# Kernel tuning notes

Hardware: AMD Instinct MI355X
Metric: run time of the kernel (lower is better)

The kernel has to match this reference:

```python
import jax, jax.numpy as jnp
import numpy as np

C_CURV = 1.0      # manifold curvature c (= k in the torch code)
EPS = 1e-15
PROJ_EPS = 1e-5   # standard Poincare ball boundary eps for manifold.proj


def _clamp_abs(x, eps=EPS):
    return jnp.maximum(jnp.abs(x), eps) * jnp.sign(x)


def setup_inputs() -> dict:
    key = jax.random.key(0)
    k1, k2, k3 = jax.random.split(key, 3)
    B, D, C = 4096, 1024, 4096
    c = C_CURV
    x = jax.random.normal(k1, (B, D), dtype=jnp.float32)
    # reset_parameters(): a ~ N(0, D^-0.5 / sqrt(c)); p ~ N(0, 0.1) clipped to norm 0.9/sqrt(c)
    a = jax.random.normal(k2, (C, D), dtype=jnp.float32) * (D ** -0.5 / c ** 0.5)
    p = jax.random.normal(k3, (C, D), dtype=jnp.float32) * 0.1
    p_norm = jnp.linalg.norm(p, axis=1, keepdims=True)
    max_norm = 0.9 / jnp.sqrt(jnp.float32(c))
    p = p * jnp.minimum(max_norm / p_norm, 1.0)
    return {"x": x, "a": a, "p": p}


def _forward(x, a, p):
    k = jnp.float32(C_CURV)
    sqrt_k = jnp.sqrt(k)

    # manifold.proj: clip x to the open ball of radius (1 - eps)/sqrt(c)
    xn = jnp.maximum(jnp.linalg.norm(x, axis=-1, keepdims=True), EPS)
    maxn = (1.0 - PROJ_EPS) / sqrt_k
    x = jnp.where(xn > maxn, x * (maxn / xn), x)

    # Rank-structured Mobius addition: diff = mobius_add(-p, x) factors as
    #   diff[b,c,:] = (A[b,c] * (-p[c]) + Bc[c] * x[b]) / den[b,c]
    x2 = jnp.sum(x * x, axis=-1)          # [B]
    p2 = jnp.sum(p * p, axis=-1)          # [C]
    px = jnp.einsum('bd,cd->bc', x, p)    # [B,C]  <p_c, x_b>
    xa = jnp.einsum('bd,cd->bc', x, a)    # [B,C]  <a_c, x_b>
    pa = jnp.sum(p * a, axis=-1)          # [C]    <p_c, a_c>
    a_norm = jnp.sqrt(jnp.sum(a * a, axis=-1))  # [C]

    A = 1.0 - 2.0 * k * px + k * x2[:, None]                       # [B,C]
    Bc = 1.0 - k * p2                                              # [C]
    den = jnp.maximum(1.0 - 2.0 * k * px + (k * k) * x2[:, None] * p2[None, :], EPS)

    diff_norm2 = jnp.maximum(
        (A * A * p2[None, :] + (Bc * Bc)[None, :] * x2[:, None] - 2.0 * A * Bc[None, :] * px)
        / (den * den), EPS)                                        # [B,C]
    sc_diff_a = (-A * pa[None, :] + Bc[None, :] * xa) / den        # [B,C], signed

    num = 2.0 * sc_diff_a
    denom = _clamp_abs((1.0 + k * diff_norm2) * a_norm[None, :])
    distance = jnp.arcsinh(sqrt_k * num / denom) / sqrt_k
    return -distance  # logits [B,C]


def reference(x, a, p):
    return _forward(x, a, p)
```

## Files before the change

kernel.cpp:

```cpp
#include <hip/hip_runtime.h>
#include <hip/hip_bf16.h>
#include <math.h>


#define EPSF 1e-15f
#define MAXN 0.99999f

constexpr int Bdim = 4096;
constexpr int Ddim = 1024;
constexpr int Cdim = 4096;

typedef __bf16 bf16x8 __attribute__((ext_vector_type(8)));
typedef float  f32x4  __attribute__((ext_vector_type(4)));
typedef unsigned short u16;

__device__ __forceinline__ u16 f2bf(float f) {
  __hip_bfloat16 h = __float2bfloat16(f);
  return *reinterpret_cast<const u16*>(&h);
}

__device__ __forceinline__ void gl_lds16(const u16* g, u16* l) {
  __builtin_amdgcn_global_load_lds(
      (const __attribute__((address_space(1))) void*)g,
      (__attribute__((address_space(3))) void*)l, 16, 0, 0);
}


__global__ __launch_bounds__(256) void prep_x(const float* __restrict__ x,
                                              u16* __restrict__ xb,
                                              float* __restrict__ x2o) {
  const int b = blockIdx.x, t = threadIdx.x;
  float4 v = ((const float4*)(x + (size_t)b * Ddim))[t];
  float s = v.x * v.x + v.y * v.y + v.z * v.z + v.w * v.w;
  __shared__ float red[4];
#pragma unroll
  for (int o = 32; o > 0; o >>= 1) s += __shfl_down(s, o);
  if ((t & 63) == 0) red[t >> 6] = s;
  __syncthreads();
  s = red[0] + red[1] + red[2] + red[3];
  float norm  = sqrtf(s);
  float xn    = fmaxf(norm, EPSF);
  float scale = (xn > MAXN) ? (MAXN / xn) : 1.0f;
  if (t == 0) x2o[b] = s * scale * scale;
  ushort4 o4;
  o4.x = f2bf(v.x * scale); o4.y = f2bf(v.y * scale);
  o4.z = f2bf(v.z * scale); o4.w = f2bf(v.w * scale);
  ((ushort4*)(xb + (size_t)b * Ddim))[t] = o4;
}

__global__ __launch_bounds__(256) void prep_pa(const float* __restrict__ a,
                                               const float* __restrict__ p,
                                               u16* __restrict__ pab,
                                               float* __restrict__ p2o,
                                               float* __restrict__ pao,
                                               float* __restrict__ ano) {
  const int c = blockIdx.x, t = threadIdx.x;
  float4 av = ((const float4*)(a + (size_t)c * Ddim))[t];
  float4 pv = ((const float4*)(p + (size_t)c * Ddim))[t];
  float sp2 = pv.x * pv.x + pv.y * pv.y + pv.z * pv.z + pv.w * pv.w;
  float spa = pv.x * av.x + pv.y * av.y + pv.z * av.z + pv.w * av.w;
  float sa2 = av.x * av.x + av.y * av.y + av.z * av.z + av.w * av.w;
  __shared__ float red[12];
#pragma unroll
  for (int o = 32; o > 0; o >>= 1) {
    sp2 += __shfl_down(sp2, o);
    spa += __shfl_down(spa, o);
    sa2 += __shfl_down(sa2, o);
  }
  if ((t & 63) == 0) { int w = t >> 6; red[w] = sp2; red[4 + w] = spa; red[8 + w] = sa2; }
  __syncthreads();
  if (t == 0) {
    p2o[c] = red[0] + red[1] + red[2] + red[3];
    pao[c] = red[4] + red[5] + red[6] + red[7];
    ano[c] = sqrtf(red[8] + red[9] + red[10] + red[11]);
  }
  const int prP = ((c >> 4) << 5) + (c & 15);
  ushort4 oa, op;
  oa.x = f2bf(av.x); oa.y = f2bf(av.y); oa.z = f2bf(av.z); oa.w = f2bf(av.w);
  op.x = f2bf(pv.x); op.y = f2bf(pv.y); op.z = f2bf(pv.z); op.w = f2bf(pv.w);
  ((ushort4*)(pab + (size_t)prP * Ddim))[t]        = op;
  ((ushort4*)(pab + (size_t)(prP + 16) * Ddim))[t] = oa;
}


#define SBAR0() __builtin_amdgcn_sched_barrier(0)
#define GATE8() asm volatile("s_waitcnt vmcnt(8)" ::: "memory")
#define GATE4() asm volatile("s_waitcnt vmcnt(4)" ::: "memory")
#define GATE0() asm volatile("s_waitcnt vmcnt(0)" ::: "memory")

__global__ __launch_bounds__(512, 2) void gemm_ep(
    const u16* __restrict__ xb, const u16* __restrict__ pab,
    const float* __restrict__ x2g, const float* __restrict__ p2g,
    const float* __restrict__ pag, const float* __restrict__ ang,
    float* __restrict__ out) {
  __shared__ u16 Xs[4][8192];
  __shared__ u16 PAs[4][8192];

  const int t = threadIdx.x;

  const int flat  = blockIdx.y * 32 + blockIdx.x;
  const int swz   = (flat & 7) * 64 + (flat >> 3);
  const int chunk = swz >> 6;
  const int local = swz & 63;
  const int bx = chunk * 4 + (local & 3);
  const int by = local >> 2;

  const int lane = t & 63;
  const int wid  = t >> 6;
  const int wr   = wid >> 2;
  const int wc   = wid & 3;

  const int r0  = t >> 2;
  const int sw8 = ((t & 3) ^ ((r0 >> 1) & 3)) * 8;
  const u16* xsrc  = xb  + (size_t)(by * 256 + r0) * Ddim + sw8;
  const u16* pasrc = pab + (size_t)(bx * 256 + r0) * Ddim + sw8;
  const int t8 = t * 8;
  const size_t half = (size_t)128 * Ddim;

  const int arow = wr * 128 + (lane & 15);
  const int brow = wc * 64  + (lane & 15);
  const int aoff = arow * 32 + (((lane >> 4) ^ ((arow >> 1) & 3)) * 8);
  const int boff = brow * 32 + (((lane >> 4) ^ ((brow >> 1) & 3)) * 8);

  f32x4 acc[8][4];
  const f32x4 zero = {0.f, 0.f, 0.f, 0.f};
#pragma unroll
  for (int m = 0; m < 8; ++m)
#pragma unroll
    for (int n = 0; n < 4; ++n) acc[m][n] = zero;

#define MROW(M, AV) do {                                                     \
    acc[M][0] = __builtin_amdgcn_mfma_f32_16x16x32_bf16(AV, bv0, acc[M][0], 0, 0, 0); \
    acc[M][1] = __builtin_amdgcn_mfma_f32_16x16x32_bf16(AV, bv1, acc[M][1], 0, 0, 0); \
    acc[M][2] = __builtin_amdgcn_mfma_f32_16x16x32_bf16(AV, bv2, acc[M][2], 0, 0, 0); \
    acc[M][3] = __builtin_amdgcn_mfma_f32_16x16x32_bf16(AV, bv3, acc[M][3], 0, 0, 0); \
  } while (0)

#define TILE(BI, DOSTAGE, GATE) do {                                  \
    GATE;                                                             \
    __builtin_amdgcn_s_barrier();                                     \
    SBAR0();                                                          \
    if (DOSTAGE) {                                                    \
      u16* Xw  = (u16*)&Xs[((BI)+3)&3][0];                            \
      u16* PAw = (u16*)&PAs[((BI)+3)&3][0];                           \
      gl_lds16(xgp,        Xw + t8);                                  \
      gl_lds16(xgp + half, Xw + 4096 + t8);                           \
      gl_lds16(pgp,        PAw + t8);                                 \
      gl_lds16(pgp + half, PAw + 4096 + t8);                          \
      xgp += 32; pgp += 32;                                           \
    }                                                                 \
    const u16* Xr  = &Xs[(BI)][0];                                    \
    const u16* PAr = &PAs[(BI)][0];                                   \
    bf16x8 bv0 = *(const bf16x8*)&PAr[boff];                          \
    bf16x8 bv1 = *(const bf16x8*)&PAr[boff + 512];                    \
    bf16x8 bv2 = *(const bf16x8*)&PAr[boff + 1024];                   \
    bf16x8 bv3 = *(const bf16x8*)&PAr[boff + 1536];                   \
    bf16x8 a0 = *(const bf16x8*)&Xr[aoff];                            \
    bf16x8 a1 = *(const bf16x8*)&Xr[aoff + 512];                      \
    bf16x8 a2 = *(const bf16x8*)&Xr[aoff + 1024];                     \
    bf16x8 a3 = *(const bf16x8*)&Xr[aoff + 1536];                     \
    asm volatile("s_waitcnt lgkmcnt(0)" ::: "memory");                \
    SBAR0();                                                          \
    __builtin_amdgcn_s_setprio(1);                                    \
    MROW(0, a0); MROW(1, a1);                                         \
    SBAR0();                                                          \
    a0 = *(const bf16x8*)&Xr[aoff + 2048];                            \
    a1 = *(const bf16x8*)&Xr[aoff + 2560];                            \
    SBAR0();                                                          \
    MROW(2, a2); MROW(3, a3);                                         \
    SBAR0();                                                          \
    a2 = *(const bf16x8*)&Xr[aoff + 3072];                            \
    a3 = *(const bf16x8*)&Xr[aoff + 3584];                            \
    SBAR0();                                                          \
    asm volatile("s_waitcnt lgkmcnt(2)" ::: "memory");                \
    SBAR0();                                                          \
    MROW(4, a0); MROW(5, a1);                                         \
    asm volatile("s_waitcnt lgkmcnt(0)" ::: "memory");                \
    SBAR0();                                                          \
    MROW(6, a2); MROW(7, a3);                                         \
    __builtin_amdgcn_s_setprio(0);                                    \
  } while (0)

#pragma unroll
  for (int T = 0; T < 3; ++T) {
    u16* Xw  = (u16*)&Xs[T][0];
    u16* PAw = (u16*)&PAs[T][0];
    gl_lds16(xsrc  + T * 32,        Xw + t8);
    gl_lds16(xsrc  + T * 32 + half, Xw + 4096 + t8);
    gl_lds16(pasrc + T * 32,        PAw + t8);
    gl_lds16(pasrc + T * 32 + half, PAw + 4096 + t8);
  }
  const u16* xgp = xsrc  + 96;
  const u16* pgp = pasrc + 96;

  for (int g = 0; g < 7; ++g) {
    TILE(0, 1, GATE8());
    TILE(1, 1, GATE8());
    TILE(2, 1, GATE8());
    TILE(3, 1, GATE8());
  }
  TILE(0, 1, GATE8());
  TILE(1, 0, GATE8());
  TILE(2, 0, GATE4());
  TILE(3, 0, GATE0());

#undef TILE
#undef MROW

#pragma unroll
  for (int m = 0; m < 8; ++m) {
    const int rl0 = by * 256 + wr * 128 + m * 16 + (lane >> 4) * 4;
    float x2r[4];
#pragma unroll
    for (int j = 0; j < 4; ++j) x2r[j] = x2g[rl0 + j];
#pragma unroll
    for (int g = 0; g < 2; ++g) {
      const int cl = (bx * 8 + wc * 2 + g) * 16 + (lane & 15);
      const float p2c = p2g[cl];
      const float pac = pag[cl];
      const float anc = ang[cl];
      const float Bcc = 1.0f - p2c;
      f32x4 px4 = acc[m][2 * g];
      f32x4 xa4 = acc[m][2 * g + 1];
#pragma unroll
      for (int j = 0; j < 4; ++j) {
        const float px = px4[j];
        const float xa = xa4[j];
        const float Av  = 1.0f - 2.0f * px + x2r[j];
        const float den = fmaxf(1.0f - 2.0f * px + x2r[j] * p2c, EPSF);
        const float dn2 = fmaxf((Av * Av * p2c + Bcc * Bcc * x2r[j] - 2.0f * Av * Bcc * px) / (den * den), EPSF);
        const float sc  = (Bcc * xa - Av * pac) / den;
        const float dv  = fmaxf((1.0f + dn2) * anc, EPSF);
        const float z   = (2.0f * sc) / dv;
        const float z2 = z * z;
        float r;
        if (z2 > 0.04f) r = asinhf(z);
        else            r = z * (1.0f - z2 * (1.0f / 6.0f) + z2 * z2 * 0.075f);
        out[(size_t)rl0 * Cdim + j * Cdim + cl] = -r;
      }
    }
  }
}

extern "C" void kernel_launch(void* const* d_in, const int* in_sizes, int n_in,
                              void* d_out, int out_size, void* d_ws, size_t ws_size,
                              hipStream_t stream) {
  const float* x = (const float*)d_in[0];
  const float* a = (const float*)d_in[1];
  const float* p = (const float*)d_in[2];
  float* out = (float*)d_out;

  char* ws = (char*)d_ws;
  u16* xb  = (u16*)(ws);
  u16* pab = (u16*)(ws + (size_t)8 * 1024 * 1024);
  float* x2 = (float*)(ws + (size_t)24 * 1024 * 1024);
  float* p2 = x2 + Bdim;
  float* pa = p2 + Cdim;
  float* an = pa + Cdim;

  prep_x <<<Bdim, 256, 0, stream>>>(x, xb, x2);
  prep_pa<<<Cdim, 256, 0, stream>>>(a, p, pab, p2, pa, an);
  gemm_ep<<<dim3(32, 16), 512, 0, stream>>>(xb, pab, x2, p2, pa, an, out);
}
```

Before: 124.6 us.

## Double-buffer LDS fragments in registers and prefetch next tile mid-compute

The GEMM main loop now keeps two register fragment sets. Halfway through each tile's MFMA sequence it loads the next tile's B fragments and first four A fragments from LDS, so LDS read latency overlaps matrix math instead of stalling at the start of each tile. The global-load gate is relaxed from vmcnt(8) to vmcnt(4), with a one-time prologue wait before the loop. Most explicit sched_barrier and lgkmcnt waits are removed, which leaves wait placement to the compiler. The cost is higher register pressure under the 512-thread, 2-block launch bound, with some risk of spills or worse compiler scheduling.

```diff
diff --git a/kernel.cpp b/kernel.cpp
--- a/kernel.cpp
+++ b/kernel.cpp
@@ -83,10 +83,12 @@
 }
 
 
-#define SBAR0() __builtin_amdgcn_sched_barrier(0)
-#define GATE8() asm volatile("s_waitcnt vmcnt(8)" ::: "memory")
-#define GATE4() asm volatile("s_waitcnt vmcnt(4)" ::: "memory")
-#define GATE0() asm volatile("s_waitcnt vmcnt(0)" ::: "memory")
+#define GATEV8() asm volatile("s_waitcnt vmcnt(8)" ::: "memory")
+#define GATEV4() asm volatile("s_waitcnt vmcnt(4)" ::: "memory")
+#define GATEV0() asm volatile("s_waitcnt vmcnt(0)" ::: "memory")
+#define GATENONE()
+
+struct Frag { bf16x8 bv[4]; bf16x8 av[4]; };
 
 __global__ __launch_bounds__(512, 2) void gemm_ep(
     const u16* __restrict__ xb, const u16* __restrict__ pab,
@@ -129,17 +131,30 @@
 #pragma unroll
     for (int n = 0; n < 4; ++n) acc[m][n] = zero;
 
-#define MROW(M, AV) do {                                                     \
-    acc[M][0] = __builtin_amdgcn_mfma_f32_16x16x32_bf16(AV, bv0, acc[M][0], 0, 0, 0); \
-    acc[M][1] = __builtin_amdgcn_mfma_f32_16x16x32_bf16(AV, bv1, acc[M][1], 0, 0, 0); \
-    acc[M][2] = __builtin_amdgcn_mfma_f32_16x16x32_bf16(AV, bv2, acc[M][2], 0, 0, 0); \
-    acc[M][3] = __builtin_amdgcn_mfma_f32_16x16x32_bf16(AV, bv3, acc[M][3], 0, 0, 0); \
+  Frag fsA, fsB;
+
+#define PREFETCH(FS, BI) do {                                         \
+    const u16* Xn  = &Xs[(BI)][0];                                    \
+    const u16* PAn = &PAs[(BI)][0];                                   \
+    _Pragma("unroll")                                                 \
+    for (int i = 0; i < 4; ++i)                                       \
+      FS.bv[i] = *(const bf16x8*)&PAn[boff + i * 512];                \
+    _Pragma("unroll")                                                 \
+    for (int i = 0; i < 4; ++i)                                       \
+      FS.av[i] = *(const bf16x8*)&Xn[aoff + i * 512];                 \
   } while (0)
 
-#define TILE(BI, DOSTAGE, GATE) do {                                  \
+#define MROW4(M, AV, FS) do {                                         \
+    acc[M][0] = __builtin_amdgcn_mfma_f32_16x16x32_bf16(AV, FS.bv[0], acc[M][0], 0, 0, 0); \
+    acc[M][1] = __builtin_amdgcn_mfma_f32_16x16x32_bf16(AV, FS.bv[1], acc[M][1], 0, 0, 0); \
+    acc[M][2] = __builtin_amdgcn_mfma_f32_16x16x32_bf16(AV, FS.bv[2], acc[M][2], 0, 0, 0); \
+    acc[M][3] = __builtin_amdgcn_mfma_f32_16x16x32_bf16(AV, FS.bv[3], acc[M][3], 0, 0, 0); \
+  } while (0)
+
+#define TILEBODY(CUR, NXT, BI, DOSTAGE, GATE, DOPREF) do {            \
     GATE;                                                             \
     __builtin_amdgcn_s_barrier();                                     \
-    SBAR0();                                                          \
+    __builtin_amdgcn_sched_barrier(0);                                \
     if (DOSTAGE) {                                                    \
       u16* Xw  = (u16*)&Xs[((BI)+3)&3][0];                            \
       u16* PAw = (u16*)&PAs[((BI)+3)&3][0];                           \
@@ -149,35 +164,19 @@
       gl_lds16(pgp + half, PAw + 4096 + t8);                          \
       xgp += 32; pgp += 32;                                           \
     }                                                                 \
-    const u16* Xr  = &Xs[(BI)][0];                                    \
-    const u16* PAr = &PAs[(BI)][0];                                   \
-    bf16x8 bv0 = *(const bf16x8*)&PAr[boff];                          \
-    bf16x8 bv1 = *(const bf16x8*)&PAr[boff + 512];                    \
-    bf16x8 bv2 = *(const bf16x8*)&PAr[boff + 1024];                   \
-    bf16x8 bv3 = *(const bf16x8*)&PAr[boff + 1536];                   \
-    bf16x8 a0 = *(const bf16x8*)&Xr[aoff];                            \
-    bf16x8 a1 = *(const bf16x8*)&Xr[aoff + 512];                      \
-    bf16x8 a2 = *(const bf16x8*)&Xr[aoff + 1024];                     \
-    bf16x8 a3 = *(const bf16x8*)&Xr[aoff + 1536];                     \
-    asm volatile("s_waitcnt lgkmcnt(0)" ::: "memory");                \
-    SBAR0();                                                          \
+    const u16* Xc = &Xs[(BI)][0];                                     \
+    bf16x8 w0 = *(const bf16x8*)&Xc[aoff + 2048];                     \
+    bf16x8 w1 = *(const bf16x8*)&Xc[aoff + 2560];                     \
+    bf16x8 w2 = *(const bf16x8*)&Xc[aoff + 3072];                     \
+    bf16x8 w3 = *(const bf16x8*)&Xc[aoff + 3584];                     \
     __builtin_amdgcn_s_setprio(1);                                    \
-    MROW(0, a0); MROW(1, a1);                                         \
-    SBAR0();                                                          \
-    a0 = *(const bf16x8*)&Xr[aoff + 2048];                            \
-    a1 = *(const bf16x8*)&Xr[aoff + 2560];                            \
-    SBAR0();                                                          \
-    MROW(2, a2); MROW(3, a3);                                         \
-    SBAR0();                                                          \
-    a2 = *(const bf16x8*)&Xr[aoff + 3072];                            \
-    a3 = *(const bf16x8*)&Xr[aoff + 3584];                            \
-    SBAR0();                                                          \
-    asm volatile("s_waitcnt lgkmcnt(2)" ::: "memory");                \
-    SBAR0();                                                          \
-    MROW(4, a0); MROW(5, a1);                                         \
-    asm volatile("s_waitcnt lgkmcnt(0)" ::: "memory");                \
-    SBAR0();                                                          \
-    MROW(6, a2); MROW(7, a3);                                         \
+    MROW4(0, CUR.av[0], CUR); MROW4(1, CUR.av[1], CUR);               \
+    MROW4(2, CUR.av[2], CUR); MROW4(3, CUR.av[3], CUR);               \
+    __builtin_amdgcn_s_setprio(0);                                    \
+    if (DOPREF) PREFETCH(NXT, ((BI)+1)&3);                            \
+    __builtin_amdgcn_s_setprio(1);                                    \
+    MROW4(4, w0, CUR); MROW4(5, w1, CUR);                             \
+    MROW4(6, w2, CUR); MROW4(7, w3, CUR);                             \
     __builtin_amdgcn_s_setprio(0);                                    \
   } while (0)
 
@@ -192,20 +191,25 @@
   }
   const u16* xgp = xsrc  + 96;
   const u16* pgp = pasrc + 96;
-
-  for (int g = 0; g < 7; ++g) {
-    TILE(0, 1, GATE8());
-    TILE(1, 1, GATE8());
-    TILE(2, 1, GATE8());
-    TILE(3, 1, GATE8());
-  }
-  TILE(0, 1, GATE8());
-  TILE(1, 0, GATE8());
-  TILE(2, 0, GATE4());
-  TILE(3, 0, GATE0());
-
-#undef TILE
-#undef MROW
+  GATEV8();
+  __builtin_amdgcn_s_barrier();
+  __builtin_amdgcn_sched_barrier(0);
+  PREFETCH(fsA, 0);
+
+  for (int gg = 0; gg < 7; ++gg) {
+    TILEBODY(fsA, fsB, 0, 1, GATEV4(), 1);
+    TILEBODY(fsB, fsA, 1, 1, GATEV4(), 1);
+    TILEBODY(fsA, fsB, 2, 1, GATEV4(), 1);
+    TILEBODY(fsB, fsA, 3, 1, GATEV4(), 1);
+  }
+  TILEBODY(fsA, fsB, 0, 1, GATEV4(), 1);
+  TILEBODY(fsB, fsA, 1, 0, GATEV4(), 1);
+  TILEBODY(fsA, fsB, 2, 0, GATEV0(), 1);
+  TILEBODY(fsB, fsA, 3, 0, GATENONE(), 0);
+
+#undef TILEBODY
+#undef PREFETCH
+#undef MROW4
 
 #pragma unroll
   for (int m = 0; m < 8; ++m) {
```

Result: no change. 127.1 us (+2.0%).

## Shrink GEMM block to 256x128 with 4 waves and triple-buffered LDS pipeline

Applied to the files above, without the earlier changes.

Moves the fused GEMM from a 256x256 tile with 8 waves and a 4-stage LDS ring to a 256x128 tile with 4 waves and a 3-stage ring, doubling the grid to 1024 blocks. The hand-interleaved LDS loads and MFMAs are replaced by a simple load-all-then-compute loop, and the epilogue uses a precomputed reciprocal of the a-norm plus hardware rcp instead of divisions. The intent is better occupancy and load balance across CUs and a cheaper epilogue. In exchange, per-block reuse of the x tile drops, global traffic rises, and the approximate reciprocals slightly change numerics.

```diff
diff --git a/kernel.cpp b/kernel.cpp
--- a/kernel.cpp
+++ b/kernel.cpp
@@ -53,7 +53,7 @@
                                                u16* __restrict__ pab,
                                                float* __restrict__ p2o,
                                                float* __restrict__ pao,
-                                               float* __restrict__ ano) {
+                                               float* __restrict__ anio) {
   const int c = blockIdx.x, t = threadIdx.x;
   float4 av = ((const float4*)(a + (size_t)c * Ddim))[t];
   float4 pv = ((const float4*)(p + (size_t)c * Ddim))[t];
@@ -70,9 +70,9 @@
   if ((t & 63) == 0) { int w = t >> 6; red[w] = sp2; red[4 + w] = spa; red[8 + w] = sa2; }
   __syncthreads();
   if (t == 0) {
-    p2o[c] = red[0] + red[1] + red[2] + red[3];
-    pao[c] = red[4] + red[5] + red[6] + red[7];
-    ano[c] = sqrtf(red[8] + red[9] + red[10] + red[11]);
+    p2o[c]  = red[0] + red[1] + red[2] + red[3];
+    pao[c]  = red[4] + red[5] + red[6] + red[7];
+    anio[c] = 1.0f / sqrtf(red[8] + red[9] + red[10] + red[11]);
   }
   const int prP = ((c >> 4) << 5) + (c & 15);
   ushort4 oa, op;
@@ -83,39 +83,34 @@
 }
 
 
-#define SBAR0() __builtin_amdgcn_sched_barrier(0)
-#define GATE8() asm volatile("s_waitcnt vmcnt(8)" ::: "memory")
-#define GATE4() asm volatile("s_waitcnt vmcnt(4)" ::: "memory")
-#define GATE0() asm volatile("s_waitcnt vmcnt(0)" ::: "memory")
-
-__global__ __launch_bounds__(512, 2) void gemm_ep(
+__global__ __launch_bounds__(256, 2) void gemm_ep(
     const u16* __restrict__ xb, const u16* __restrict__ pab,
     const float* __restrict__ x2g, const float* __restrict__ p2g,
-    const float* __restrict__ pag, const float* __restrict__ ang,
+    const float* __restrict__ pag, const float* __restrict__ anig,
     float* __restrict__ out) {
-  __shared__ u16 Xs[4][8192];
-  __shared__ u16 PAs[4][8192];
+  __shared__ u16 Xs[3][8192];
+  __shared__ u16 PAs[3][4096];
 
   const int t = threadIdx.x;
 
-  const int flat  = blockIdx.y * 32 + blockIdx.x;
-  const int swz   = (flat & 7) * 64 + (flat >> 3);
-  const int chunk = swz >> 6;
-  const int local = swz & 63;
-  const int bx = chunk * 4 + (local & 3);
-  const int by = local >> 2;
+  const int flat  = blockIdx.y * 64 + blockIdx.x;
+  const int swz   = (flat & 7) * 128 + (flat >> 3);
+  const int chunk = swz >> 7;
+  const int local = swz & 127;
+  const int by = chunk * 2 + (local >> 6);
+  const int bx = local & 63;
 
   const int lane = t & 63;
   const int wid  = t >> 6;
-  const int wr   = wid >> 2;
-  const int wc   = wid & 3;
+  const int wr   = wid >> 1;
+  const int wc   = wid & 1;
 
   const int r0  = t >> 2;
   const int sw8 = ((t & 3) ^ ((r0 >> 1) & 3)) * 8;
   const u16* xsrc  = xb  + (size_t)(by * 256 + r0) * Ddim + sw8;
-  const u16* pasrc = pab + (size_t)(bx * 256 + r0) * Ddim + sw8;
+  const u16* pasrc = pab + (size_t)(bx * 128 + r0) * Ddim + sw8;
   const int t8 = t * 8;
-  const size_t half = (size_t)128 * Ddim;
+  const size_t q64 = (size_t)64 * Ddim;
 
   const int arow = wr * 128 + (lane & 15);
   const int brow = wc * 64  + (lane & 15);
@@ -129,28 +124,21 @@
 #pragma unroll
     for (int n = 0; n < 4; ++n) acc[m][n] = zero;
 
-#define MROW(M, AV) do {                                                     \
-    acc[M][0] = __builtin_amdgcn_mfma_f32_16x16x32_bf16(AV, bv0, acc[M][0], 0, 0, 0); \
-    acc[M][1] = __builtin_amdgcn_mfma_f32_16x16x32_bf16(AV, bv1, acc[M][1], 0, 0, 0); \
-    acc[M][2] = __builtin_amdgcn_mfma_f32_16x16x32_bf16(AV, bv2, acc[M][2], 0, 0, 0); \
-    acc[M][3] = __builtin_amdgcn_mfma_f32_16x16x32_bf16(AV, bv3, acc[M][3], 0, 0, 0); \
+#define STAGE(SLOT) do {                                              \
+    u16* Xw  = (u16*)&Xs[(SLOT)][0];                                  \
+    u16* PAw = (u16*)&PAs[(SLOT)][0];                                 \
+    gl_lds16(xgp,            Xw + t8);                                \
+    gl_lds16(xgp + q64,      Xw + 2048 + t8);                         \
+    gl_lds16(xgp + 2 * q64,  Xw + 4096 + t8);                         \
+    gl_lds16(xgp + 3 * q64,  Xw + 6144 + t8);                         \
+    gl_lds16(pgp,            PAw + t8);                               \
+    gl_lds16(pgp + q64,      PAw + 2048 + t8);                        \
+    xgp += 32; pgp += 32;                                             \
   } while (0)
 
-#define TILE(BI, DOSTAGE, GATE) do {                                  \
-    GATE;                                                             \
-    __builtin_amdgcn_s_barrier();                                     \
-    SBAR0();                                                          \
-    if (DOSTAGE) {                                                    \
-      u16* Xw  = (u16*)&Xs[((BI)+3)&3][0];                            \
-      u16* PAw = (u16*)&PAs[((BI)+3)&3][0];                           \
-      gl_lds16(xgp,        Xw + t8);                                  \
-      gl_lds16(xgp + half, Xw + 4096 + t8);                           \
-      gl_lds16(pgp,        PAw + t8);                                 \
-      gl_lds16(pgp + half, PAw + 4096 + t8);                          \
-      xgp += 32; pgp += 32;                                           \
-    }                                                                 \
-    const u16* Xr  = &Xs[(BI)][0];                                    \
-    const u16* PAr = &PAs[(BI)][0];                                   \
+#define COMPUTE(SLOT) do {                                            \
+    const u16* Xr  = &Xs[(SLOT)][0];                                  \
+    const u16* PAr = &PAs[(SLOT)][0];                                 \
     bf16x8 bv0 = *(const bf16x8*)&PAr[boff];                          \
     bf16x8 bv1 = *(const bf16x8*)&PAr[boff + 512];                    \
     bf16x8 bv2 = *(const bf16x8*)&PAr[boff + 1024];                   \
@@ -159,66 +147,60 @@
     bf16x8 a1 = *(const bf16x8*)&Xr[aoff + 512];                      \
     bf16x8 a2 = *(const bf16x8*)&Xr[aoff + 1024];                     \
     bf16x8 a3 = *(const bf16x8*)&Xr[aoff + 1536];                     \
-    asm volatile("s_waitcnt lgkmcnt(0)" ::: "memory");                \
-    SBAR0();                                                          \
+    bf16x8 a4 = *(const bf16x8*)&Xr[aoff + 2048];                     \
+    bf16x8 a5 = *(const bf16x8*)&Xr[aoff + 2560];                     \
+    bf16x8 a6 = *(const bf16x8*)&Xr[aoff + 3072];                     \
+    bf16x8 a7 = *(const bf16x8*)&Xr[aoff + 3584];                     \
     __builtin_amdgcn_s_setprio(1);                                    \
-    MROW(0, a0); MROW(1, a1);                                         \
-    SBAR0();                                                          \
-    a0 = *(const bf16x8*)&Xr[aoff + 2048];                            \
-    a1 = *(const bf16x8*)&Xr[aoff + 2560];                            \
-    SBAR0();                                                          \
-    MROW(2, a2); MROW(3, a3);                                         \
-    SBAR0();                                                          \
-    a2 = *(const bf16x8*)&Xr[aoff + 3072];                            \
-    a3 = *(const bf16x8*)&Xr[aoff + 3584];                            \
-    SBAR0();                                                          \
-    asm volatile("s_waitcnt lgkmcnt(2)" ::: "memory");                \
-    SBAR0();                                                          \
-    MROW(4, a0); MROW(5, a1);                                         \
-    asm volatile("s_waitcnt lgkmcnt(0)" ::: "memory");                \
-    SBAR0();                                                          \
-    MROW(6, a2); MROW(7, a3);                                         \
+    _Pragma("unroll")                                                 \
+    for (int n = 0; n < 4; ++n) {                                     \
+      bf16x8 bv = (n == 0) ? bv0 : (n == 1) ? bv1 : (n == 2) ? bv2 : bv3; \
+      acc[0][n] = __builtin_amdgcn_mfma_f32_16x16x32_bf16(a0, bv, acc[0][n], 0, 0, 0); \
+      acc[1][n] = __builtin_amdgcn_mfma_f32_16x16x32_bf16(a1, bv, acc[1][n], 0, 0, 0); \
+      acc[2][n] = __builtin_amdgcn_mfma_f32_16x16x32_bf16(a2, bv, acc[2][n], 0, 0, 0); \
+      acc[3][n] = __builtin_amdgcn_mfma_f32_16x16x32_bf16(a3, bv, acc[3][n], 0, 0, 0); \
+      acc[4][n] = __builtin_amdgcn_mfma_f32_16x16x32_bf16(a4, bv, acc[4][n], 0, 0, 0); \
+      acc[5][n] = __builtin_amdgcn_mfma_f32_16x16x32_bf16(a5, bv, acc[5][n], 0, 0, 0); \
+      acc[6][n] = __builtin_amdgcn_mfma_f32_16x16x32_bf16(a6, bv, acc[6][n], 0, 0, 0); \
+      acc[7][n] = __builtin_amdgcn_mfma_f32_16x16x32_bf16(a7, bv, acc[7][n], 0, 0, 0); \
+    }                                                                 \
     __builtin_amdgcn_s_setprio(0);                                    \
   } while (0)
 
-#pragma unroll
-  for (int T = 0; T < 3; ++T) {
-    u16* Xw  = (u16*)&Xs[T][0];
-    u16* PAw = (u16*)&PAs[T][0];
-    gl_lds16(xsrc  + T * 32,        Xw + t8);
-    gl_lds16(xsrc  + T * 32 + half, Xw + 4096 + t8);
-    gl_lds16(pasrc + T * 32,        PAw + t8);
-    gl_lds16(pasrc + T * 32 + half, PAw + 4096 + t8);
-  }
-  const u16* xgp = xsrc  + 96;
-  const u16* pgp = pasrc + 96;
-
-  for (int g = 0; g < 7; ++g) {
-    TILE(0, 1, GATE8());
-    TILE(1, 1, GATE8());
-    TILE(2, 1, GATE8());
-    TILE(3, 1, GATE8());
-  }
-  TILE(0, 1, GATE8());
-  TILE(1, 0, GATE8());
-  TILE(2, 0, GATE4());
-  TILE(3, 0, GATE0());
-
-#undef TILE
-#undef MROW
+#define GATE_BAR(N) do {                                              \
+    asm volatile("s_waitcnt vmcnt(" #N ")" ::: "memory");             \
+    __builtin_amdgcn_s_barrier();                                     \
+    __builtin_amdgcn_sched_barrier(0);                                \
+  } while (0)
+
+  const u16* xgp = xsrc;
+  const u16* pgp = pasrc;
+  STAGE(0);
+  STAGE(1);
+
+  for (int g = 0; g < 10; ++g) {
+    GATE_BAR(6);  STAGE(2);  COMPUTE(0);
+    GATE_BAR(6);  STAGE(0);  COMPUTE(1);
+    GATE_BAR(6);  STAGE(1);  COMPUTE(2);
+  }
+  GATE_BAR(6);  COMPUTE(0);
+  GATE_BAR(0);  COMPUTE(1);
+
+#undef GATE_BAR
+#undef STAGE
+#undef COMPUTE
 
 #pragma unroll
   for (int m = 0; m < 8; ++m) {
     const int rl0 = by * 256 + wr * 128 + m * 16 + (lane >> 4) * 4;
-    float x2r[4];
-#pragma unroll
-    for (int j = 0; j < 4; ++j) x2r[j] = x2g[rl0 + j];
+    const float4 x2r4 = *(const float4*)&x2g[rl0];
+    float x2r[4] = {x2r4.x, x2r4.y, x2r4.z, x2r4.w};
 #pragma unroll
     for (int g = 0; g < 2; ++g) {
-      const int cl = (bx * 8 + wc * 2 + g) * 16 + (lane & 15);
+      const int cl = bx * 64 + wc * 32 + g * 16 + (lane & 15);
       const float p2c = p2g[cl];
       const float pac = pag[cl];
-      const float anc = ang[cl];
+      const float ani = anig[cl];
       const float Bcc = 1.0f - p2c;
       f32x4 px4 = acc[m][2 * g];
       f32x4 xa4 = acc[m][2 * g + 1];
@@ -226,12 +208,12 @@
       for (int j = 0; j < 4; ++j) {
         const float px = px4[j];
         const float xa = xa4[j];
-        const float Av  = 1.0f - 2.0f * px + x2r[j];
-        const float den = fmaxf(1.0f - 2.0f * px + x2r[j] * p2c, EPSF);
-        const float dn2 = fmaxf((Av * Av * p2c + Bcc * Bcc * x2r[j] - 2.0f * Av * Bcc * px) / (den * den), EPSF);
-        const float sc  = (Bcc * xa - Av * pac) / den;
-        const float dv  = fmaxf((1.0f + dn2) * anc, EPSF);
-        const float z   = (2.0f * sc) / dv;
+        const float Av   = 1.0f - 2.0f * px + x2r[j];
+        const float den  = fmaxf(1.0f - 2.0f * px + x2r[j] * p2c, EPSF);
+        const float rden = __builtin_amdgcn_rcpf(den);
+        const float dn2  = fmaxf((Av * Av * p2c + Bcc * Bcc * x2r[j] - 2.0f * Av * Bcc * px) * rden * rden, EPSF);
+        const float sc   = (Bcc * xa - Av * pac) * rden;
+        const float z    = 2.0f * sc * ani * __builtin_amdgcn_rcpf(1.0f + dn2);
         const float z2 = z * z;
         float r;
         if (z2 > 0.04f) r = asinhf(z);
@@ -253,12 +235,12 @@
   char* ws = (char*)d_ws;
   u16* xb  = (u16*)(ws);
   u16* pab = (u16*)(ws + (size_t)8 * 1024 * 1024);
-  float* x2 = (float*)(ws + (size_t)24 * 1024 * 1024);
-  float* p2 = x2 + Bdim;
-  float* pa = p2 + Cdim;
-  float* an = pa + Cdim;
+  float* x2  = (float*)(ws + (size_t)24 * 1024 * 1024);
+  float* p2  = x2 + Bdim;
+  float* pa  = p2 + Cdim;
+  float* ani = pa + Cdim;
 
   prep_x <<<Bdim, 256, 0, stream>>>(x, xb, x2);
-  prep_pa<<<Cdim, 256, 0, stream>>>(a, p, pab, p2, pa, an);
-  gemm_ep<<<dim3(32, 16), 512, 0, stream>>>(xb, pab, x2, p2, pa, an, out);
-}
+  prep_pa<<<Cdim, 256, 0, stream>>>(a, p, pab, p2, pa, ani);
+  gemm_ep<<<dim3(64, 16), 256, 0, stream>>>(xb, pab, x2, p2, pa, ani, out);
+}
```

Result: faster. 110.9 us (-11.0%).
